# Optimization experiments

Measured on AMD Instinct MI355X. Metric: run time of the kernel, lower is better.

Reference implementation:

```python
import jax, jax.numpy as jnp
import numpy as np

D_IN, D_H, D_OUT = 1024, 1024, 1024
D_MOE = 4096
N_EXPERTS = 8
TOP_K = 2


def setup_inputs() -> dict:
    key = jax.random.key(0)
    ks = jax.random.split(key, 10)
    s = lambda d: 1.0 / np.sqrt(d)
    x = jax.random.normal(ks[0], (2, 2048, D_IN), dtype=jnp.float32)
    W_in = jax.random.normal(ks[1], (D_IN, D_H), dtype=jnp.float32) * s(D_IN)
    b_in = jnp.zeros((D_H,), jnp.float32)
    W_gate = jax.random.normal(ks[2], (D_H, N_EXPERTS), dtype=jnp.float32) * s(D_H)
    b_gate = jnp.zeros((N_EXPERTS,), jnp.float32)
    W1 = jax.random.normal(ks[3], (N_EXPERTS, D_H, D_MOE), dtype=jnp.float32) * s(D_H)
    b1 = jnp.zeros((N_EXPERTS, D_MOE), jnp.float32)
    W2 = jax.random.normal(ks[4], (N_EXPERTS, D_MOE, D_H), dtype=jnp.float32) * s(D_MOE)
    b2 = jnp.zeros((N_EXPERTS, D_H), jnp.float32)
    W_out = jax.random.normal(ks[5], (D_H, D_OUT), dtype=jnp.float32) * s(D_H)
    b_out = jnp.zeros((D_OUT,), jnp.float32)
    return {"x": x, "W_in": W_in, "b_in": b_in, "W_gate": W_gate, "b_gate": b_gate,
            "W1": W1, "b1": b1, "W2": W2, "b2": b2, "W_out": W_out, "b_out": b_out}


def reference(x, W_in, b_in, W_gate, b_gate, W1, b1, W2, b2, W_out, b_out):
    B, S, _ = x.shape
    h = x @ W_in + b_in                       # [B,S,D_H]
    t = h.reshape(B * S, -1)                  # tokens [N,D_H]

    # --- top-k softmax gating ---
    logits = t @ W_gate + b_gate              # [N,E]
    probs = jax.nn.softmax(logits, axis=-1)
    topv, topi = jax.lax.top_k(probs, TOP_K)  # [N,k]
    topv = topv / jnp.sum(topv, axis=-1, keepdims=True)
    # dense routing weights [N,E] (zeros for unselected experts)
    route = jnp.zeros_like(probs).at[jnp.arange(t.shape[0])[:, None], topi].set(topv)

    # --- expert MLPs (dense all-expert compute, weighted combine) ---
    mid = jax.nn.relu(jnp.einsum('nd,edh->neh', t, W1) + b1)   # [N,E,D_MOE]
    eout = jnp.einsum('neh,ehd->ned', mid, W2) + b2            # [N,E,D_H]
    moe_out = jnp.einsum('ne,ned->nd', route, eout)            # [N,D_H]

    out = moe_out.reshape(B, S, -1) @ W_out + b_out            # [B,S,D_OUT]
    return out
```

## Files before the change

kernel.cpp:

```cpp
#include <hip/hip_runtime.h>
#include <hip/hip_bf16.h>

typedef __bf16 bf16_t;
typedef bf16_t bf16x8 __attribute__((ext_vector_type(8)));
typedef bf16_t bf16x4 __attribute__((ext_vector_type(4)));
typedef float f32x4 __attribute__((ext_vector_type(4)));

#define DIN 1024
#define DH 1024
#define DMOE 4096
#define NEXP 8
#define NTOK 4096

__device__ __forceinline__ void gload_lds16(const bf16_t* g, bf16_t* l) {
  __builtin_amdgcn_global_load_lds(
      (const __attribute__((address_space(1))) void*)g,
      (__attribute__((address_space(3))) void*)l, 16, 0, 0);
}

__global__ void k_prep_all(const float* __restrict__ W_in, const float* __restrict__ W1,
                           const float* __restrict__ W2, const float* __restrict__ W_out,
                           const float* __restrict__ x,
                           const float* __restrict__ Wgate, const float* __restrict__ b_in,
                           const float* __restrict__ b_gate,
                           bf16_t* __restrict__ WtIn, bf16_t* __restrict__ Wt1,
                           bf16_t* __restrict__ Wt2, bf16_t* __restrict__ WtOut,
                           bf16_t* __restrict__ xbf,
                           double* __restrict__ G, double* __restrict__ cvec,
                           int* __restrict__ cnt) {
  const int z = blockIdx.x;
  if (z >= 20992) {
    const int b = z - 20992;
    if (b == 0 && threadIdx.x < 8) cnt[threadIdx.x] = 0;
    const int lane = threadIdx.x & 63;
    const int wave = b * 4 + (threadIdx.x >> 6);
    const int nw = 256;
    for (int d = wave; d <= DIN; d += nw) {
      const float* row = (d < DIN) ? (W_in + (size_t)d * DH) : b_in;
      double acc[8] = {0, 0, 0, 0, 0, 0, 0, 0};
      for (int k = lane; k < DH; k += 64) {
        const double xv = (double)row[k];
        const float* g = Wgate + (size_t)k * NEXP;
#pragma unroll
        for (int ee = 0; ee < 8; ++ee) acc[ee] += xv * (double)g[ee];
      }
#pragma unroll
      for (int ee = 0; ee < 8; ++ee) {
        double a = acc[ee];
        for (int o = 32; o > 0; o >>= 1) a += __shfl_down(a, o);
        acc[ee] = a;
      }
      if (lane == 0) {
        if (d < DIN) {
#pragma unroll
          for (int ee = 0; ee < 8; ++ee) G[(size_t)d * 8 + ee] = acc[ee];
        } else {
#pragma unroll
          for (int ee = 0; ee < 8; ++ee) cvec[ee] = acc[ee] + (double)b_gate[ee];
        }
      }
    }
    return;
  }
  if (z >= 16896) {
    const int i = (z - 16896) * 256 + threadIdx.x;
    const float4 v = *(const float4*)(x + (size_t)i * 4);
    bf16x4 o;
    o.x = (bf16_t)v.x; o.y = (bf16_t)v.y; o.z = (bf16_t)v.z; o.w = (bf16_t)v.w;
    *(bf16x4*)(xbf + (size_t)i * 4) = o;
    return;
  }
  const float* s; bf16_t* d; int R, C, tx, ty;
  if (z < 256) {
    s = W_in; d = WtIn; R = DIN; C = DH; tx = z & 15; ty = z >> 4;
  } else if (z < 8448) {
    const int l = z - 256, e = l >> 10, t = l & 1023;
    s = W1 + (size_t)e * DH * DMOE; d = Wt1 + (size_t)e * DH * DMOE;
    R = DH; C = DMOE; tx = t & 63; ty = t >> 6;
  } else if (z < 16640) {
    const int l = z - 8448, e = l >> 10, t = l & 1023;
    s = W2 + (size_t)e * DMOE * DH; d = Wt2 + (size_t)e * DMOE * DH;
    R = DMOE; C = DH; tx = t & 15; ty = t >> 4;
  } else {
    const int t = z - 16640;
    s = W_out; d = WtOut; R = DH; C = DH; tx = t & 15; ty = t >> 4;
  }
  __shared__ float tile[64][65];
  const int c0 = tx * 64, r0 = ty * 64;
  const int t = threadIdx.x;
  const int rr = t >> 4;
  const int cc = (t & 15) << 2;
#pragma unroll
  for (int i = 0; i < 64; i += 16) {
    const float4 v = *(const float4*)&s[(size_t)(r0 + rr + i) * C + c0 + cc];
    tile[rr + i][cc + 0] = v.x;
    tile[rr + i][cc + 1] = v.y;
    tile[rr + i][cc + 2] = v.z;
    tile[rr + i][cc + 3] = v.w;
  }
  __syncthreads();
  const int orr = (t & 7) * 8;
  const int oc = t >> 3;
#pragma unroll
  for (int i = 0; i < 64; i += 32) {
    bf16x8 o;
#pragma unroll
    for (int j = 0; j < 8; ++j) o[j] = (bf16_t)tile[orr + j][oc + i];
    *(bf16x8*)&d[(size_t)(c0 + oc + i) * R + r0 + orr] = o;
  }
}

__global__ void k_combine(const bf16_t* __restrict__ eout, bf16_t* __restrict__ moebf) {
  const int i = blockIdx.x * blockDim.x + threadIdx.x;
  const int t = i >> 8;
  const int q = (i & 255) * 4;
  const bf16x4 a = *(const bf16x4*)(eout + ((size_t)t * 2) * DH + q);
  const bf16x4 b = *(const bf16x4*)(eout + ((size_t)t * 2 + 1) * DH + q);
  bf16x4 o;
  o.x = (bf16_t)((float)a.x + (float)b.x);
  o.y = (bf16_t)((float)a.y + (float)b.y);
  o.z = (bf16_t)((float)a.z + (float)b.z);
  o.w = (bf16_t)((float)a.w + (float)b.w);
  *(bf16x4*)(moebf + (size_t)t * DH + q) = o;
}

__global__ __launch_bounds__(256, 3) void k_gemm0_gating(
    const bf16_t* __restrict__ A, const bf16_t* __restrict__ B,
    const float* __restrict__ bias, bf16_t* __restrict__ Cbase,
    const float* __restrict__ x, const double* __restrict__ G,
    const double* __restrict__ cvec, int* __restrict__ cnt,
    int* __restrict__ list, float* __restrict__ wlist) {
  constexpr int M = NTOK, N = DH, K = DIN;
  if (blockIdx.z > 0) {
    const int lane = threadIdx.x & 63;
    const int bl = (blockIdx.z - 1) * 256 + blockIdx.y * 8 + blockIdx.x;
    const int t = bl * 4 + (threadIdx.x >> 6);
    const float* xr = x + (size_t)t * DIN;
    double acc[8] = {0, 0, 0, 0, 0, 0, 0, 0};
    for (int d = lane; d < DIN; d += 64) {
      const double xv = (double)xr[d];
      const double* g = G + (size_t)d * 8;
#pragma unroll
      for (int ee = 0; ee < 8; ++ee) acc[ee] += xv * g[ee];
    }
#pragma unroll
    for (int ee = 0; ee < 8; ++ee) {
      double a = acc[ee];
      for (int o = 32; o > 0; o >>= 1) a += __shfl_down(a, o);
      acc[ee] = a;
    }
    if (lane == 0) {
      double l[8];
#pragma unroll
      for (int ee = 0; ee < 8; ++ee) l[ee] = acc[ee] + cvec[ee];
      double m = l[0];
#pragma unroll
      for (int ee = 1; ee < 8; ++ee) m = fmax(m, l[ee]);
      double p[8];
#pragma unroll
      for (int ee = 0; ee < 8; ++ee) p[ee] = exp(l[ee] - m);
      int i1 = 0;
#pragma unroll
      for (int ee = 1; ee < 8; ++ee)
        if (p[ee] > p[i1]) i1 = ee;
      int i2 = (i1 == 0) ? 1 : 0;
#pragma unroll
      for (int ee = 0; ee < 8; ++ee)
        if (ee != i1 && p[ee] > p[i2]) i2 = ee;
      const double s2 = p[i1] + p[i2];
      const float w1 = (float)(p[i1] / s2);
      const float w2 = (float)(p[i2] / s2);
      int lp = atomicAdd(&cnt[i1], 1);
      list[i1 * NTOK + lp] = t * 2;
      wlist[i1 * NTOK + lp] = w1;
      lp = atomicAdd(&cnt[i2], 1);
      list[i2 * NTOK + lp] = t * 2 + 1;
      wlist[i2 * NTOK + lp] = w2;
    }
    return;
  }

  const int mblk = blockIdx.y, nblk = blockIdx.x;

  __shared__ bf16_t As[3][128 * 32];
  __shared__ bf16_t Bs[3][128 * 32];

  const int tid = threadIdx.x;
  const int lane = tid & 63;
  const int wid = tid >> 6;
  const int wr = wid >> 1, wc = wid & 1;

  const int srow0 = wid * 32 + (lane >> 2);
  const int srow1 = srow0 + 16;
  const int skcol = ((lane & 3) ^ ((lane >> 3) & 3)) * 8;

  const bf16_t* aptr0 = A + (size_t)(mblk * 128 + srow0) * K + skcol;
  const bf16_t* aptr1 = A + (size_t)(mblk * 128 + srow1) * K + skcol;
  const bf16_t* bptr0 = B + (size_t)(nblk * 128 + srow0) * K + skcol;
  const bf16_t* bptr1 = B + (size_t)(nblk * 128 + srow1) * K + skcol;

  const int ldsOfsA0 = (wid * 32) * 32;
  const int ldsOfsA1 = (wid * 32 + 16) * 32;

  f32x4 acc[4][4] = {};
  const int nkt = K >> 5;

  auto stage = [&](int buf, int kt) {
    const size_t ko = (size_t)kt * 32;
    gload_lds16(aptr0 + ko, &As[buf][ldsOfsA0]);
    gload_lds16(aptr1 + ko, &As[buf][ldsOfsA1]);
    gload_lds16(bptr0 + ko, &Bs[buf][ldsOfsA0]);
    gload_lds16(bptr1 + ko, &Bs[buf][ldsOfsA1]);
  };

  stage(0, 0);
  if (nkt > 1) stage(1, 1);

  const int fr = lane & 15;
  const int s0 = (((lane >> 4) ^ ((fr >> 1) & 3)) << 3);

  int cur = 0;
  for (int kt = 0; kt < nkt; ++kt) {
    int nxt = cur + 2;
    if (nxt >= 3) nxt -= 3;
    if (kt + 2 < nkt) {
      stage(nxt, kt + 2);
      asm volatile("s_waitcnt vmcnt(8)" ::: "memory");
    } else if (kt + 1 < nkt) {
      asm volatile("s_waitcnt vmcnt(4)" ::: "memory");
    } else {
      asm volatile("s_waitcnt vmcnt(0)" ::: "memory");
    }
    __builtin_amdgcn_s_barrier();

    bf16x8 af[4], bfr[4];
#pragma unroll
    for (int m = 0; m < 4; ++m)
      af[m] = *(const bf16x8*)&As[cur][(wr * 64 + m * 16 + fr) * 32 + s0];
#pragma unroll
    for (int n = 0; n < 4; ++n)
      bfr[n] = *(const bf16x8*)&Bs[cur][(wc * 64 + n * 16 + fr) * 32 + s0];
#pragma unroll
    for (int m = 0; m < 4; ++m)
#pragma unroll
      for (int n = 0; n < 4; ++n)
        acc[m][n] = __builtin_amdgcn_mfma_f32_16x16x32_bf16(af[m], bfr[n], acc[m][n], 0, 0, 0);

    __builtin_amdgcn_s_barrier();
    cur += 1;
    if (cur >= 3) cur -= 3;
  }

  const int colBase = nblk * 128 + wc * 64 + (lane & 15);
  const int rowBase = mblk * 128 + wr * 64 + ((lane >> 4) << 2);
#pragma unroll
  for (int n = 0; n < 4; ++n) {
    const int c = colBase + n * 16;
    const float bv = bias[c];
#pragma unroll
    for (int m = 0; m < 4; ++m) {
#pragma unroll
      for (int j = 0; j < 4; ++j) {
        const int r = rowBase + m * 16 + j;
        Cbase[(size_t)r * N + c] = (bf16_t)(acc[m][n][j] + bv);
      }
    }
  }
}

__global__ __launch_bounds__(256, 3) void k_gemm_out(
    const bf16_t* __restrict__ A, const bf16_t* __restrict__ B,
    const float* __restrict__ bias, float* __restrict__ Cbase,
    int M, int N, int K) {
  const int mblk = blockIdx.y, nblk = blockIdx.x;

  __shared__ bf16_t As[3][128 * 32];
  __shared__ bf16_t Bs[3][128 * 32];

  const int tid = threadIdx.x;
  const int lane = tid & 63;
  const int wid = tid >> 6;
  const int wr = wid >> 1, wc = wid & 1;

  const int srow0 = wid * 32 + (lane >> 2);
  const int srow1 = srow0 + 16;
  const int skcol = ((lane & 3) ^ ((lane >> 3) & 3)) * 8;

  const bf16_t* aptr0 = A + (size_t)(mblk * 128 + srow0) * K + skcol;
  const bf16_t* aptr1 = A + (size_t)(mblk * 128 + srow1) * K + skcol;
  const bf16_t* bptr0 = B + (size_t)(nblk * 128 + srow0) * K + skcol;
  const bf16_t* bptr1 = B + (size_t)(nblk * 128 + srow1) * K + skcol;

  const int ldsOfsA0 = (wid * 32) * 32;
  const int ldsOfsA1 = (wid * 32 + 16) * 32;

  f32x4 acc[4][4] = {};
  const int nkt = K >> 5;

  auto stage = [&](int buf, int kt) {
    const size_t ko = (size_t)kt * 32;
    gload_lds16(aptr0 + ko, &As[buf][ldsOfsA0]);
    gload_lds16(aptr1 + ko, &As[buf][ldsOfsA1]);
    gload_lds16(bptr0 + ko, &Bs[buf][ldsOfsA0]);
    gload_lds16(bptr1 + ko, &Bs[buf][ldsOfsA1]);
  };

  stage(0, 0);
  if (nkt > 1) stage(1, 1);

  const int fr = lane & 15;
  const int s0 = (((lane >> 4) ^ ((fr >> 1) & 3)) << 3);

  int cur = 0;
  for (int kt = 0; kt < nkt; ++kt) {
    int nxt = cur + 2;
    if (nxt >= 3) nxt -= 3;
    if (kt + 2 < nkt) {
      stage(nxt, kt + 2);
      asm volatile("s_waitcnt vmcnt(8)" ::: "memory");
    } else if (kt + 1 < nkt) {
      asm volatile("s_waitcnt vmcnt(4)" ::: "memory");
    } else {
      asm volatile("s_waitcnt vmcnt(0)" ::: "memory");
    }
    __builtin_amdgcn_s_barrier();

    bf16x8 af[4], bfr[4];
#pragma unroll
    for (int m = 0; m < 4; ++m)
      af[m] = *(const bf16x8*)&As[cur][(wr * 64 + m * 16 + fr) * 32 + s0];
#pragma unroll
    for (int n = 0; n < 4; ++n)
      bfr[n] = *(const bf16x8*)&Bs[cur][(wc * 64 + n * 16 + fr) * 32 + s0];
#pragma unroll
    for (int m = 0; m < 4; ++m)
#pragma unroll
      for (int n = 0; n < 4; ++n)
        acc[m][n] = __builtin_amdgcn_mfma_f32_16x16x32_bf16(af[m], bfr[n], acc[m][n], 0, 0, 0);

    __builtin_amdgcn_s_barrier();
    cur += 1;
    if (cur >= 3) cur -= 3;
  }

  const int colBase = nblk * 128 + wc * 64 + (lane & 15);
  const int rowBase = mblk * 128 + wr * 64 + ((lane >> 4) << 2);
#pragma unroll
  for (int n = 0; n < 4; ++n) {
    const int c = colBase + n * 16;
    const float bv = bias[c];
#pragma unroll
    for (int m = 0; m < 4; ++m) {
#pragma unroll
      for (int j = 0; j < 4; ++j) {
        const int r = rowBase + m * 16 + j;
        Cbase[(size_t)r * N + c] = acc[m][n][j] + bv;
      }
    }
  }
}

__global__ __launch_bounds__(512, 4) void k_gemm1(
    const bf16_t* __restrict__ Abase, const bf16_t* __restrict__ Bbase,
    const float* __restrict__ biasBase, bf16_t* __restrict__ Cbase,
    int N, int K,
    const int* __restrict__ cnt, const int* __restrict__ listBase) {
  const int e = blockIdx.z;
  const int mblk = blockIdx.y, nblk = blockIdx.x;
  const int Mloc = cnt[e];
  if (mblk * 256 >= Mloc) return;
  int rowOff = 0;
  for (int i = 0; i < NEXP; ++i) rowOff += (i < e) ? cnt[i] : 0;
  const bf16_t* B = Bbase + (size_t)e * N * K;
  const float* bias = biasBase + (size_t)e * N;
  const int* myList = listBase + e * NTOK;

  __shared__ bf16_t As[3][256 * 32];
  __shared__ bf16_t Bs[3][128 * 32];

  const int tid = threadIdx.x;
  const int lane = tid & 63;
  const int wid = tid >> 6;
  const int wr = wid >> 1, wc = wid & 1;

  const int subr = lane >> 2;
  const int skcol = ((lane & 3) ^ ((lane >> 3) & 3)) * 8;

  uint32_t aofs[2];
#pragma unroll
  for (int l = 0; l < 2; ++l) {
    int ar = mblk * 256 + (wid * 2 + l) * 16 + subr;
    if (ar > Mloc - 1) ar = Mloc - 1;
    aofs[l] = (uint32_t)(myList[ar] >> 1) * (uint32_t)K + skcol;
  }
  const uint32_t bofs = (uint32_t)(nblk * 128 + wid * 16 + subr) * (uint32_t)K + skcol;

  f32x4 acc[4][4] = {};
  const int nkt = K >> 5;

  auto stage = [&](int buf, int kt) {
    const uint32_t ko = (uint32_t)kt * 32;
    gload_lds16(Abase + aofs[0] + ko, &As[buf][(wid * 2 + 0) * 512]);
    gload_lds16(Abase + aofs[1] + ko, &As[buf][(wid * 2 + 1) * 512]);
    gload_lds16(B + bofs + ko, &Bs[buf][wid * 512]);
  };

  stage(0, 0);
  if (nkt > 1) stage(1, 1);

  const int fr = lane & 15;
  const int s0 = (((lane >> 4) ^ ((fr >> 1) & 3)) << 3);

  int cur = 0;
  for (int kt = 0; kt < nkt; ++kt) {
    int nxt = cur + 2;
    if (nxt >= 3) nxt -= 3;
    if (kt + 2 < nkt) {
      stage(nxt, kt + 2);
      asm volatile("s_waitcnt vmcnt(6)" ::: "memory");
    } else if (kt + 1 < nkt) {
      asm volatile("s_waitcnt vmcnt(3)" ::: "memory");
    } else {
      asm volatile("s_waitcnt vmcnt(0)" ::: "memory");
    }
    __builtin_amdgcn_s_barrier();

    bf16x8 af[4], bfr[4];
#pragma unroll
    for (int m = 0; m < 4; ++m)
      af[m] = *(const bf16x8*)&As[cur][(wr * 64 + m * 16 + fr) * 32 + s0];
#pragma unroll
    for (int n = 0; n < 4; ++n)
      bfr[n] = *(const bf16x8*)&Bs[cur][(wc * 64 + n * 16 + fr) * 32 + s0];
#pragma unroll
    for (int m = 0; m < 4; ++m)
#pragma unroll
      for (int n = 0; n < 4; ++n)
        acc[m][n] = __builtin_amdgcn_mfma_f32_16x16x32_bf16(af[m], bfr[n], acc[m][n], 0, 0, 0);

    __builtin_amdgcn_s_barrier();
    cur += 1;
    if (cur >= 3) cur -= 3;
  }

  const int colBase = nblk * 128 + wc * 64 + (lane & 15);
  const int rowBase = mblk * 256 + wr * 64 + ((lane >> 4) << 2);
#pragma unroll
  for (int n = 0; n < 4; ++n) {
    const int c = colBase + n * 16;
    const float bv = bias[c];
#pragma unroll
    for (int m = 0; m < 4; ++m) {
#pragma unroll
      for (int j = 0; j < 4; ++j) {
        const int r = rowBase + m * 16 + j;
        if (r < Mloc) {
          Cbase[(size_t)(rowOff + r) * N + c] = (bf16_t)fmaxf(acc[m][n][j] + bv, 0.0f);
        }
      }
    }
  }
}

__global__ __launch_bounds__(256, 3) void k_gemm_e2(
    const bf16_t* __restrict__ Abase, const bf16_t* __restrict__ Bbase,
    const float* __restrict__ biasBase, bf16_t* __restrict__ Cbase,
    int N, int K,
    const int* __restrict__ cnt, const int* __restrict__ listBase,
    const float* __restrict__ wlistBase) {
  const int e = blockIdx.z;
  const int mblk = blockIdx.y, nblk = blockIdx.x;
  const int Mloc = cnt[e];
  if (mblk * 128 >= Mloc) return;
  int rowOff = 0;
  for (int i = 0; i < NEXP; ++i) rowOff += (i < e) ? cnt[i] : 0;
  const bf16_t* B = Bbase + (size_t)e * N * K;
  const float* bias = biasBase + (size_t)e * N;
  const int* myList = listBase + e * NTOK;
  const float* myW = wlistBase + e * NTOK;
  const bf16_t* A = Abase + (size_t)rowOff * K;

  __shared__ bf16_t As[3][128 * 32];
  __shared__ bf16_t Bs[3][128 * 32];

  const int tid = threadIdx.x;
  const int lane = tid & 63;
  const int wid = tid >> 6;
  const int wr = wid >> 1, wc = wid & 1;

  const int srow0 = wid * 32 + (lane >> 2);
  const int srow1 = srow0 + 16;
  const int skcol = ((lane & 3) ^ ((lane >> 3) & 3)) * 8;

  int ar0 = mblk * 128 + srow0;
  int ar1 = mblk * 128 + srow1;
  if (ar0 > Mloc - 1) ar0 = Mloc - 1;
  if (ar1 > Mloc - 1) ar1 = Mloc - 1;
  const bf16_t* aptr0 = A + (size_t)ar0 * K + skcol;
  const bf16_t* aptr1 = A + (size_t)ar1 * K + skcol;
  const bf16_t* bptr0 = B + (size_t)(nblk * 128 + srow0) * K + skcol;
  const bf16_t* bptr1 = B + (size_t)(nblk * 128 + srow1) * K + skcol;

  const int ldsOfsA0 = (wid * 32) * 32;
  const int ldsOfsA1 = (wid * 32 + 16) * 32;

  f32x4 acc[4][4] = {};
  const int nkt = K >> 5;

  auto stage = [&](int buf, int kt) {
    const size_t ko = (size_t)kt * 32;
    gload_lds16(aptr0 + ko, &As[buf][ldsOfsA0]);
    gload_lds16(aptr1 + ko, &As[buf][ldsOfsA1]);
    gload_lds16(bptr0 + ko, &Bs[buf][ldsOfsA0]);
    gload_lds16(bptr1 + ko, &Bs[buf][ldsOfsA1]);
  };

  stage(0, 0);
  if (nkt > 1) stage(1, 1);

  const int fr = lane & 15;
  const int s0 = (((lane >> 4) ^ ((fr >> 1) & 3)) << 3);

  int cur = 0;
  for (int kt = 0; kt < nkt; ++kt) {
    int nxt = cur + 2;
    if (nxt >= 3) nxt -= 3;
    if (kt + 2 < nkt) {
      stage(nxt, kt + 2);
      asm volatile("s_waitcnt vmcnt(8)" ::: "memory");
    } else if (kt + 1 < nkt) {
      asm volatile("s_waitcnt vmcnt(4)" ::: "memory");
    } else {
      asm volatile("s_waitcnt vmcnt(0)" ::: "memory");
    }
    __builtin_amdgcn_s_barrier();

    bf16x8 af[4], bfr[4];
#pragma unroll
    for (int m = 0; m < 4; ++m)
      af[m] = *(const bf16x8*)&As[cur][(wr * 64 + m * 16 + fr) * 32 + s0];
#pragma unroll
    for (int n = 0; n < 4; ++n)
      bfr[n] = *(const bf16x8*)&Bs[cur][(wc * 64 + n * 16 + fr) * 32 + s0];
#pragma unroll
    for (int m = 0; m < 4; ++m)
#pragma unroll
      for (int n = 0; n < 4; ++n)
        acc[m][n] = __builtin_amdgcn_mfma_f32_16x16x32_bf16(af[m], bfr[n], acc[m][n], 0, 0, 0);

    __builtin_amdgcn_s_barrier();
    cur += 1;
    if (cur >= 3) cur -= 3;
  }

  const int colBase = nblk * 128 + wc * 64 + (lane & 15);
  const int rowBase = mblk * 128 + wr * 64 + ((lane >> 4) << 2);
#pragma unroll
  for (int n = 0; n < 4; ++n) {
    const int c = colBase + n * 16;
    const float bv = bias[c];
#pragma unroll
    for (int m = 0; m < 4; ++m) {
#pragma unroll
      for (int j = 0; j < 4; ++j) {
        const int r = rowBase + m * 16 + j;
        if (r < Mloc) {
          const int entry = myList[r];
          const float w = myW[r];
          Cbase[(size_t)entry * DH + c] = (bf16_t)((acc[m][n][j] + bv) * w);
        }
      }
    }
  }
}


extern "C" void kernel_launch(void* const* d_in, const int* in_sizes, int n_in,
                              void* d_out, int out_size, void* d_ws, size_t ws_size,
                              hipStream_t stream) {
  const float* x      = (const float*)d_in[0];
  const float* W_in   = (const float*)d_in[1];
  const float* b_in   = (const float*)d_in[2];
  const float* W_gate = (const float*)d_in[3];
  const float* b_gate = (const float*)d_in[4];
  const float* W1     = (const float*)d_in[5];
  const float* b1     = (const float*)d_in[6];
  const float* W2     = (const float*)d_in[7];
  const float* b2     = (const float*)d_in[8];
  const float* W_out  = (const float*)d_in[9];
  const float* b_out  = (const float*)d_in[10];

  char* ws = (char*)d_ws;
  size_t off = 0;
  auto alloc = [&](size_t bytes) -> void* {
    void* p = ws + off;
    off += (bytes + 255) & ~(size_t)255;
    return p;
  };

  bf16_t* WtIn  = (bf16_t*)alloc((size_t)DH * DIN * 2);
  bf16_t* Wt1   = (bf16_t*)alloc((size_t)NEXP * DMOE * DH * 2);
  bf16_t* Wt2   = (bf16_t*)alloc((size_t)NEXP * DH * DMOE * 2);
  bf16_t* WtOut = (bf16_t*)alloc((size_t)DH * DH * 2);
  bf16_t* xbf   = (bf16_t*)alloc((size_t)NTOK * DIN * 2);
  bf16_t* hbf   = (bf16_t*)alloc((size_t)NTOK * DH * 2);
  bf16_t* mid   = (bf16_t*)alloc((size_t)2 * NTOK * DMOE * 2);
  bf16_t* eoutb = (bf16_t*)alloc((size_t)2 * NTOK * DH * 2);
  bf16_t* moebf = (bf16_t*)alloc((size_t)NTOK * DH * 2);
  double* G     = (double*)alloc((size_t)DIN * 8 * 8);
  double* cvec  = (double*)alloc(8 * 8);
  int*    cnt   = (int*)alloc(NEXP * 4);
  int*    list  = (int*)alloc((size_t)NEXP * NTOK * 4);
  float*  wlist = (float*)alloc((size_t)NEXP * NTOK * 4);

  k_prep_all<<<21056, 256, 0, stream>>>(W_in, W1, W2, W_out, x, W_gate, b_in, b_gate,
                                        WtIn, Wt1, Wt2, WtOut, xbf, G, cvec, cnt);

  k_gemm0_gating<<<dim3(DH / 128, NTOK / 128, 5), 256, 0, stream>>>(
      xbf, WtIn, b_in, hbf, x, G, cvec, cnt, list, wlist);

  k_gemm1<<<dim3(DMOE / 128, NTOK / 256, NEXP), 512, 0, stream>>>(
      hbf, Wt1, b1, mid, DMOE, DH, cnt, list);
  k_gemm_e2<<<dim3(DH / 128, NTOK / 128, NEXP), 256, 0, stream>>>(
      mid, Wt2, b2, eoutb, DH, DMOE, cnt, list, wlist);
  k_combine<<<NTOK * DH / 4 / 256, 256, 0, stream>>>(eoutb, moebf);
  k_gemm_out<<<dim3(DH / 128, NTOK / 128, 1), 256, 0, stream>>>(
      moebf, WtOut, b_out, (float*)d_out, NTOK, DH, DH);
}
```

Baseline: 528.5 us.

## Overlap expert weight transposes with first GEMM and gating in one launch

Splits the prep kernel so only W_in transpose, x conversion and gate-matrix precompute run first. The large W1/W2/W_out fp32-to-bf16 transposes move into extra grid z-slices of the first GEMM+gating kernel, so this bandwidth-bound work can run alongside the compute-bound GEMM. The cost is a bigger grid and shared LDS reuse for transpose blocks. Transpose blocks may also be scheduled ahead of the GEMM blocks and delay them.

```diff
diff --git a/kernel.cpp b/kernel.cpp
--- a/kernel.cpp
+++ b/kernel.cpp
@@ -18,74 +18,10 @@
       (__attribute__((address_space(3))) void*)l, 16, 0, 0);
 }
 
-__global__ void k_prep_all(const float* __restrict__ W_in, const float* __restrict__ W1,
-                           const float* __restrict__ W2, const float* __restrict__ W_out,
-                           const float* __restrict__ x,
-                           const float* __restrict__ Wgate, const float* __restrict__ b_in,
-                           const float* __restrict__ b_gate,
-                           bf16_t* __restrict__ WtIn, bf16_t* __restrict__ Wt1,
-                           bf16_t* __restrict__ Wt2, bf16_t* __restrict__ WtOut,
-                           bf16_t* __restrict__ xbf,
-                           double* __restrict__ G, double* __restrict__ cvec,
-                           int* __restrict__ cnt) {
-  const int z = blockIdx.x;
-  if (z >= 20992) {
-    const int b = z - 20992;
-    if (b == 0 && threadIdx.x < 8) cnt[threadIdx.x] = 0;
-    const int lane = threadIdx.x & 63;
-    const int wave = b * 4 + (threadIdx.x >> 6);
-    const int nw = 256;
-    for (int d = wave; d <= DIN; d += nw) {
-      const float* row = (d < DIN) ? (W_in + (size_t)d * DH) : b_in;
-      double acc[8] = {0, 0, 0, 0, 0, 0, 0, 0};
-      for (int k = lane; k < DH; k += 64) {
-        const double xv = (double)row[k];
-        const float* g = Wgate + (size_t)k * NEXP;
-#pragma unroll
-        for (int ee = 0; ee < 8; ++ee) acc[ee] += xv * (double)g[ee];
-      }
-#pragma unroll
-      for (int ee = 0; ee < 8; ++ee) {
-        double a = acc[ee];
-        for (int o = 32; o > 0; o >>= 1) a += __shfl_down(a, o);
-        acc[ee] = a;
-      }
-      if (lane == 0) {
-        if (d < DIN) {
-#pragma unroll
-          for (int ee = 0; ee < 8; ++ee) G[(size_t)d * 8 + ee] = acc[ee];
-        } else {
-#pragma unroll
-          for (int ee = 0; ee < 8; ++ee) cvec[ee] = acc[ee] + (double)b_gate[ee];
-        }
-      }
-    }
-    return;
-  }
-  if (z >= 16896) {
-    const int i = (z - 16896) * 256 + threadIdx.x;
-    const float4 v = *(const float4*)(x + (size_t)i * 4);
-    bf16x4 o;
-    o.x = (bf16_t)v.x; o.y = (bf16_t)v.y; o.z = (bf16_t)v.z; o.w = (bf16_t)v.w;
-    *(bf16x4*)(xbf + (size_t)i * 4) = o;
-    return;
-  }
-  const float* s; bf16_t* d; int R, C, tx, ty;
-  if (z < 256) {
-    s = W_in; d = WtIn; R = DIN; C = DH; tx = z & 15; ty = z >> 4;
-  } else if (z < 8448) {
-    const int l = z - 256, e = l >> 10, t = l & 1023;
-    s = W1 + (size_t)e * DH * DMOE; d = Wt1 + (size_t)e * DH * DMOE;
-    R = DH; C = DMOE; tx = t & 63; ty = t >> 6;
-  } else if (z < 16640) {
-    const int l = z - 8448, e = l >> 10, t = l & 1023;
-    s = W2 + (size_t)e * DMOE * DH; d = Wt2 + (size_t)e * DMOE * DH;
-    R = DMOE; C = DH; tx = t & 15; ty = t >> 4;
-  } else {
-    const int t = z - 16640;
-    s = W_out; d = WtOut; R = DH; C = DH; tx = t & 15; ty = t >> 4;
-  }
-  __shared__ float tile[64][65];
+__device__ __forceinline__ void transpose_tile(const float* __restrict__ s,
+                                               bf16_t* __restrict__ d, int R, int C,
+                                               int tx, int ty, void* smem) {
+  float (*tile)[65] = (float(*)[65])smem;
   const int c0 = tx * 64, r0 = ty * 64;
   const int t = threadIdx.x;
   const int rr = t >> 4;
@@ -107,6 +43,57 @@
 #pragma unroll
     for (int j = 0; j < 8; ++j) o[j] = (bf16_t)tile[orr + j][oc + i];
     *(bf16x8*)&d[(size_t)(c0 + oc + i) * R + r0 + orr] = o;
+  }
+}
+
+__global__ void k_prep_small(const float* __restrict__ W_in, const float* __restrict__ x,
+                             const float* __restrict__ Wgate, const float* __restrict__ b_in,
+                             const float* __restrict__ b_gate,
+                             bf16_t* __restrict__ WtIn, bf16_t* __restrict__ xbf,
+                             double* __restrict__ G, double* __restrict__ cvec,
+                             int* __restrict__ cnt) {
+  const int z = blockIdx.x;
+  if (z < 256) {
+    __shared__ float tile[64][65];
+    transpose_tile(W_in, WtIn, DIN, DH, z & 15, z >> 4, tile);
+    return;
+  }
+  if (z < 4352) {
+    const int i = (z - 256) * 256 + threadIdx.x;
+    const float4 v = *(const float4*)(x + (size_t)i * 4);
+    bf16x4 o;
+    o.x = (bf16_t)v.x; o.y = (bf16_t)v.y; o.z = (bf16_t)v.z; o.w = (bf16_t)v.w;
+    *(bf16x4*)(xbf + (size_t)i * 4) = o;
+    return;
+  }
+  const int b = z - 4352;
+  if (b == 0 && threadIdx.x < 8) cnt[threadIdx.x] = 0;
+  const int lane = threadIdx.x & 63;
+  const int wave = b * 4 + (threadIdx.x >> 6);
+  for (int d = wave; d <= DIN; d += 256) {
+    const float* row = (d < DIN) ? (W_in + (size_t)d * DH) : b_in;
+    double acc[8] = {0, 0, 0, 0, 0, 0, 0, 0};
+    for (int k = lane; k < DH; k += 64) {
+      const double xv = (double)row[k];
+      const float* g = Wgate + (size_t)k * NEXP;
+#pragma unroll
+      for (int ee = 0; ee < 8; ++ee) acc[ee] += xv * (double)g[ee];
+    }
+#pragma unroll
+    for (int ee = 0; ee < 8; ++ee) {
+      double a = acc[ee];
+      for (int o = 32; o > 0; o >>= 1) a += __shfl_down(a, o);
+      acc[ee] = a;
+    }
+    if (lane == 0) {
+      if (d < DIN) {
+#pragma unroll
+        for (int ee = 0; ee < 8; ++ee) G[(size_t)d * 8 + ee] = acc[ee];
+      } else {
+#pragma unroll
+        for (int ee = 0; ee < 8; ++ee) cvec[ee] = acc[ee] + (double)b_gate[ee];
+      }
+    }
   }
 }
 
@@ -124,13 +111,37 @@
   *(bf16x4*)(moebf + (size_t)t * DH + q) = o;
 }
 
-__global__ __launch_bounds__(256, 3) void k_gemm0_gating(
+__global__ __launch_bounds__(256, 3) void k_mega(
     const bf16_t* __restrict__ A, const bf16_t* __restrict__ B,
     const float* __restrict__ bias, bf16_t* __restrict__ Cbase,
     const float* __restrict__ x, const double* __restrict__ G,
     const double* __restrict__ cvec, int* __restrict__ cnt,
-    int* __restrict__ list, float* __restrict__ wlist) {
-  constexpr int M = NTOK, N = DH, K = DIN;
+    int* __restrict__ list, float* __restrict__ wlist,
+    const float* __restrict__ W1, const float* __restrict__ W2,
+    const float* __restrict__ W_out,
+    bf16_t* __restrict__ Wt1, bf16_t* __restrict__ Wt2, bf16_t* __restrict__ WtOut) {
+  constexpr int N = DH, K = DIN;
+
+  __shared__ bf16_t As[3][128 * 32];
+  __shared__ bf16_t Bs[3][128 * 32];
+
+  if (blockIdx.z >= 5) {
+    const int t6 = (blockIdx.z - 5) * 256 + blockIdx.y * 8 + blockIdx.x;
+    if (t6 < 8192) {
+      const int e = t6 >> 10, tt = t6 & 1023;
+      transpose_tile(W1 + (size_t)e * DH * DMOE, Wt1 + (size_t)e * DH * DMOE,
+                     DH, DMOE, tt & 63, tt >> 6, As);
+    } else if (t6 < 16384) {
+      const int l = t6 - 8192, e = l >> 10, tt = l & 1023;
+      transpose_tile(W2 + (size_t)e * DMOE * DH, Wt2 + (size_t)e * DMOE * DH,
+                     DMOE, DH, tt & 15, tt >> 4, As);
+    } else {
+      const int tt = t6 - 16384;
+      transpose_tile(W_out, WtOut, DH, DH, tt & 15, tt >> 4, As);
+    }
+    return;
+  }
+
   if (blockIdx.z > 0) {
     const int lane = threadIdx.x & 63;
     const int bl = (blockIdx.z - 1) * 256 + blockIdx.y * 8 + blockIdx.x;
@@ -181,9 +192,6 @@
   }
 
   const int mblk = blockIdx.y, nblk = blockIdx.x;
-
-  __shared__ bf16_t As[3][128 * 32];
-  __shared__ bf16_t Bs[3][128 * 32];
 
   const int tid = threadIdx.x;
   const int lane = tid & 63;
@@ -613,11 +621,12 @@
   int*    list  = (int*)alloc((size_t)NEXP * NTOK * 4);
   float*  wlist = (float*)alloc((size_t)NEXP * NTOK * 4);
 
-  k_prep_all<<<21056, 256, 0, stream>>>(W_in, W1, W2, W_out, x, W_gate, b_in, b_gate,
-                                        WtIn, Wt1, Wt2, WtOut, xbf, G, cvec, cnt);
-
-  k_gemm0_gating<<<dim3(DH / 128, NTOK / 128, 5), 256, 0, stream>>>(
-      xbf, WtIn, b_in, hbf, x, G, cvec, cnt, list, wlist);
+  k_prep_small<<<4416, 256, 0, stream>>>(W_in, x, W_gate, b_in, b_gate,
+                                         WtIn, xbf, G, cvec, cnt);
+
+  k_mega<<<dim3(DH / 128, NTOK / 128, 70), 256, 0, stream>>>(
+      xbf, WtIn, b_in, hbf, x, G, cvec, cnt, list, wlist,
+      W1, W2, W_out, Wt1, Wt2, WtOut);
 
   k_gemm1<<<dim3(DMOE / 128, NTOK / 256, NEXP), 512, 0, stream>>>(
       hbf, Wt1, b1, mid, DMOE, DH, cnt, list);
```

After: 514.5 us. 1.03x faster.
